# Kernel optimization log

Measured on AMD Instinct MI355X. Metric: run time of the kernel, lower is better.

The kernel has to match this reference:

```python
import jax, jax.numpy as jnp
import numpy as np

# The external iir2d op is a channel-wise separable 2D recursive IIR filter.
# Canonical reference semantics: first-order causal+anticausal recurrence applied
# along W then H:  y[t] = (1-a)*x[t] + a*y[t-1], with 'mirror' border handled by
# initializing the carry with the edge sample (y[0] = x[0]).
# filter_id selects the feedback coefficient a.
FID_TO_A = {1: 0.1, 3: 0.3, 4: 0.4, 8: 0.8}
FILTER_IDS = (1, 3, 4, 8)


def _iir_axis(x, a, axis):
    """Causal then anticausal first-order IIR along `axis` (mirror border)."""
    xm = jnp.moveaxis(x, axis, 0)

    def step(c, xt):
        y = (1.0 - a) * xt + a * c
        return y, y

    _, yf = jax.lax.scan(step, xm[0], xm)          # causal pass
    yr = yf[::-1]
    _, yb = jax.lax.scan(step, yr[0], yr)          # anticausal pass
    return jnp.moveaxis(yb[::-1], 0, axis)


def _iir2d_nhwc(x, a):
    # Channel-wise separable 2D IIR: along W (axis 2) then H (axis 1).
    return _iir_axis(_iir_axis(x, a, 2), a, 1)


def setup_inputs() -> dict:
    key = jax.random.key(0)
    kx, kg = jax.random.split(key)
    N, H, W, C = 4, 256, 256, 96
    x = jax.random.normal(kx, (N, H, W, C), dtype=jnp.float32)
    gate_logits = jax.random.normal(kg, (len(FILTER_IDS), C), dtype=jnp.float32)
    return {"x": x, "gate_logits": gate_logits}


def reference(x, gate_logits):
    # softmax over the filter axis, broadcast as (F,1,1,1,C)
    weights = jax.nn.softmax(gate_logits, axis=0).reshape(
        (len(FILTER_IDS), 1, 1, 1, -1))
    ys = [_iir2d_nhwc(x, FID_TO_A[fid]) for fid in FILTER_IDS]
    stacked = jnp.stack(ys, axis=0)               # (F, N, H, W, C)
    return jnp.sum(stacked * weights, axis=0)      # (N, H, W, C)
```

## Files before the change

kernel.cpp:

```cpp
#include <hip/hip_runtime.h>
#include <hip/hip_fp16.h>

#define N_ 4
#define H_ 256
#define W_ 256
#define C_ 96
#define CH 48
#define NC4 12
#define TP 258
#define SP 132
#define NFILT 4

__constant__ float c_a[NFILT] = {0.1f, 0.3f, 0.4f, 0.8f};

__device__ __forceinline__ void scan_fwd(float &v0, float &v1, float &v2, float &v3,
                                         float a, int lane) {
  const float b = 1.0f - a;
  const float a2 = a * a, a3 = a2 * a, a4 = a2 * a2;
  float t0 = b * v0;
  float t1 = fmaf(a, t0, b * v1);
  float t2 = fmaf(a, t1, b * v2);
  float t3 = fmaf(a, t2, b * v3);
  if (lane == 0) {
    t0 = fmaf(a,  v0, t0);
    t1 = fmaf(a2, v0, t1);
    t2 = fmaf(a3, v0, t2);
    t3 = fmaf(a4, v0, t3);
  }
  float c = t3;
  float m = a4;
  #pragma unroll
  for (int d = 1; d <= 8; d <<= 1) {
    float o = __shfl_up(c, (unsigned)d, 64);
    if (lane >= d) c = fmaf(m, o, c);
    m = m * m;
  }
  float cin = __shfl_up(c, 1u, 64);
  if (lane == 0) cin = 0.0f;
  v0 = fmaf(a,  cin, t0);
  v1 = fmaf(a2, cin, t1);
  v2 = fmaf(a3, cin, t2);
  v3 = fmaf(a4, cin, t3);
}

__device__ __forceinline__ void scan_bwd(float &v0, float &v1, float &v2, float &v3,
                                         float a, int lane) {
  const float b = 1.0f - a;
  const float a2 = a * a, a3 = a2 * a, a4 = a2 * a2;
  float t3 = b * v3;
  float t2 = fmaf(a, t3, b * v2);
  float t1 = fmaf(a, t2, b * v1);
  float t0 = fmaf(a, t1, b * v0);
  if (lane == 63) {
    t3 = fmaf(a,  v3, t3);
    t2 = fmaf(a2, v3, t2);
    t1 = fmaf(a3, v3, t1);
    t0 = fmaf(a4, v3, t0);
  }
  float c = t0;
  float m = a4;
  #pragma unroll
  for (int d = 1; d <= 8; d <<= 1) {
    float o = __shfl_down(c, (unsigned)d, 64);
    if (lane < 64 - d) c = fmaf(m, o, c);
    m = m * m;
  }
  float cin = __shfl_down(c, 1u, 64);
  if (lane == 63) cin = 0.0f;
  v3 = fmaf(a,  cin, t3);
  v2 = fmaf(a2, cin, t2);
  v1 = fmaf(a3, cin, t1);
  v0 = fmaf(a4, cin, t0);
}

__global__ __launch_bounds__(256, 4)
void k_wpass(const float* __restrict__ x, __half* __restrict__ inter,
             int f_start, int nf) {
  __shared__ __half tile[CH * TP];
  const int chalf = blockIdx.x;
  const int row   = blockIdx.y;
  const int h     = row & 255;
  const int c0    = chalf * CH;
  const int t     = threadIdx.x;
  const int wave  = t >> 6, lane = t & 63;

  const float* xrow = x + (size_t)row * (W_ * C_) + c0;
  #pragma unroll
  for (int i = 0; i < 12; ++i) {
    int idx = t + i * 256;
    int w = idx / NC4, c4 = idx % NC4;
    const float4 v = *(const float4*)(xrow + (size_t)w * C_ + 4 * c4);
    tile[(4 * c4 + 0) * TP + w] = __float2half(v.x);
    tile[(4 * c4 + 1) * TP + w] = __float2half(v.y);
    tile[(4 * c4 + 2) * TP + w] = __float2half(v.z);
    tile[(4 * c4 + 3) * TP + w] = __float2half(v.w);
  }
  __syncthreads();

  float xf[NC4][4];
  #pragma unroll
  for (int ci = 0; ci < NC4; ++ci) {
    const int c = wave + 4 * ci;
    const __half2* p = (const __half2*)(tile + c * TP + 4 * lane);
    float2 f01 = __half22float2(p[0]);
    float2 f23 = __half22float2(p[1]);
    xf[ci][0] = f01.x; xf[ci][1] = f01.y;
    xf[ci][2] = f23.x; xf[ci][3] = f23.y;
  }

  for (int fi = 0; fi < nf; ++fi) {
    const float a = c_a[f_start + fi];
    #pragma unroll
    for (int ci = 0; ci < NC4; ++ci) {
      float v0 = xf[ci][0], v1 = xf[ci][1], v2 = xf[ci][2], v3 = xf[ci][3];
      scan_fwd(v0, v1, v2, v3, a, lane);
      scan_bwd(v0, v1, v2, v3, a, lane);
      const int c = wave + 4 * ci;
      __half2* p = (__half2*)(tile + c * TP + 4 * lane);
      p[0] = __floats2half2_rn(v0, v1);
      p[1] = __floats2half2_rn(v2, v3);
    }
    __syncthreads();
    __half* ibase = inter + (((size_t)(fi * 2 + chalf) * N_ * W_ + (size_t)(row >> 8) * W_)
                             * (H_ * CH)) + (size_t)h * CH;
    #pragma unroll
    for (int i = 0; i < 6; ++i) {
      int idx = t + i * 256;
      int w = idx / 6, j = idx % 6;
      union { uint4 u; ushort s[8]; } pk;
      #pragma unroll
      for (int k = 0; k < 8; ++k)
        pk.s[k] = __half_as_ushort(tile[(8 * j + k) * TP + w]);
      *(uint4*)(ibase + (size_t)w * (H_ * CH) + 8 * j) = pk.u;
    }
    if (fi + 1 < nf) __syncthreads();
  }
}

__global__ __launch_bounds__(256, 4)
void k_hpass(const __half* __restrict__ inter, const float* __restrict__ gate,
             float* __restrict__ out, int f_start, int nf, int accumulate) {
  __shared__ __align__(16) unsigned char smem[CH * SP * 4];
  __half* tile = (__half*)smem;
  float*  stage = (float*)smem;
  __shared__ float wlds[NFILT * CH];
  const int chalf = blockIdx.x;
  const int col   = blockIdx.y;
  const int n = col >> 8, w = col & 255;
  const int c0 = chalf * CH;
  const int t = threadIdx.x;
  const int wave = t >> 6, lane = t & 63;

  if (t < CH) {
    const int c = c0 + t;
    float g0 = gate[0 * C_ + c], g1 = gate[1 * C_ + c];
    float g2 = gate[2 * C_ + c], g3 = gate[3 * C_ + c];
    float mx = fmaxf(fmaxf(g0, g1), fmaxf(g2, g3));
    float e0 = __expf(g0 - mx), e1 = __expf(g1 - mx);
    float e2 = __expf(g2 - mx), e3 = __expf(g3 - mx);
    float inv = 1.0f / (e0 + e1 + e2 + e3);
    wlds[0 * CH + t] = e0 * inv;
    wlds[1 * CH + t] = e1 * inv;
    wlds[2 * CH + t] = e2 * inv;
    wlds[3 * CH + t] = e3 * inv;
  }

  float acc[NC4][4];
  #pragma unroll
  for (int ci = 0; ci < NC4; ++ci)
    acc[ci][0] = acc[ci][1] = acc[ci][2] = acc[ci][3] = 0.0f;

  const size_t chunk = (size_t)H_ * CH;
  uint4 pf[6];
  {
    const uint4* src = (const uint4*)(inter +
        ((size_t)(0 * 2 + chalf) * N_ * W_ + (size_t)n * W_ + w) * chunk);
    #pragma unroll
    for (int i = 0; i < 6; ++i) pf[i] = src[i * 256 + t];
  }

  for (int fi = 0; fi < nf; ++fi) {
    __syncthreads();
    #pragma unroll
    for (int i = 0; i < 6; ++i) {
      int e = i * 256 + t;
      int h = e / 6, c8 = e % 6;
      union { uint4 u; ushort s[8]; } pk;
      pk.u = pf[i];
      #pragma unroll
      for (int k = 0; k < 8; ++k)
        tile[(8 * c8 + k) * TP + h] = __ushort_as_half(pk.s[k]);
    }
    __syncthreads();
    if (fi + 1 < nf) {
      const uint4* src = (const uint4*)(inter +
          ((size_t)((fi + 1) * 2 + chalf) * N_ * W_ + (size_t)n * W_ + w) * chunk);
      #pragma unroll
      for (int i = 0; i < 6; ++i) pf[i] = src[i * 256 + t];
    }
    const float a = c_a[f_start + fi];
    #pragma unroll
    for (int ci = 0; ci < NC4; ++ci) {
      const int c = wave + 4 * ci;
      const __half2* p = (const __half2*)(tile + c * TP + 4 * lane);
      float2 f01 = __half22float2(p[0]);
      float2 f23 = __half22float2(p[1]);
      float v0 = f01.x, v1 = f01.y, v2 = f23.x, v3 = f23.y;
      scan_fwd(v0, v1, v2, v3, a, lane);
      scan_bwd(v0, v1, v2, v3, a, lane);
      const float wg = wlds[(f_start + fi) * CH + c];
      acc[ci][0] = fmaf(wg, v0, acc[ci][0]);
      acc[ci][1] = fmaf(wg, v1, acc[ci][1]);
      acc[ci][2] = fmaf(wg, v2, acc[ci][2]);
      acc[ci][3] = fmaf(wg, v3, acc[ci][3]);
    }
  }

  #pragma unroll
  for (int r = 0; r < 2; ++r) {
    __syncthreads();
    if ((lane >> 5) == r) {
      const int hl = 4 * (lane & 31);
      #pragma unroll
      for (int ci = 0; ci < NC4; ++ci) {
        float4* sp = (float4*)(stage + (wave + 4 * ci) * SP + hl);
        *sp = make_float4(acc[ci][0], acc[ci][1], acc[ci][2], acc[ci][3]);
      }
    }
    __syncthreads();
    float* obase = out + (((size_t)n * H_ + 128 * r) * W_ + w) * C_ + c0;
    #pragma unroll
    for (int i = 0; i < 6; ++i) {
      int idx = t + i * 256;
      int hl = idx / NC4, c4 = idx % NC4;
      float4 v;
      v.x = stage[(4 * c4 + 0) * SP + hl];
      v.y = stage[(4 * c4 + 1) * SP + hl];
      v.z = stage[(4 * c4 + 2) * SP + hl];
      v.w = stage[(4 * c4 + 3) * SP + hl];
      float4* dst = (float4*)(obase + (size_t)hl * (W_ * C_) + 4 * c4);
      if (accumulate) {
        float4 pv = *dst;
        v.x += pv.x; v.y += pv.y; v.z += pv.z; v.w += pv.w;
      }
      *dst = v;
    }
  }
}

extern "C" void kernel_launch(void* const* d_in, const int* in_sizes, int n_in,
                              void* d_out, int out_size, void* d_ws, size_t ws_size,
                              hipStream_t stream) {
  const float* x    = (const float*)d_in[0];
  const float* gate = (const float*)d_in[1];
  float* out        = (float*)d_out;
  __half* inter     = (__half*)d_ws;

  const size_t per_f = (size_t)N_ * H_ * W_ * C_ * sizeof(__half);
  int batch = 1;
  if (ws_size >= 4 * per_f)      batch = 4;
  else if (ws_size >= 2 * per_f) batch = 2;

  int done = 0;
  while (done < NFILT) {
    int nf = NFILT - done;
    if (nf > batch) nf = batch;
    dim3 g1(2, N_ * H_);
    k_wpass<<<g1, dim3(256), 0, stream>>>(x, inter, done, nf);
    dim3 g2(2, N_ * W_);
    k_hpass<<<g2, dim3(256), 0, stream>>>(inter, gate, out, done, nf,
                                          done > 0 ? 1 : 0);
    done += nf;
  }
}
```

Measured before the change: 349.2 us.

## Split channels into quarter blocks and double-buffer LDS tile in W pass

Blocks now cover 24 channels instead of 48, so the grid doubles and each thread holds half as many register fragments, which should raise occupancy and parallelism. The workspace layout changes to four channel chunks per filter. In the W pass the LDS tile is double-buffered by filter index, which removes the trailing barrier between filters. A duplicate clean backward scan is added and used, while the original scan_bwd is left with a strange dead expression. Smaller blocks mean more redundant per-block setup, such as the gate softmax, and shorter contiguous global transactions.

```diff
diff --git a/kernel.cpp b/kernel.cpp
--- a/kernel.cpp
+++ b/kernel.cpp
@@ -5,8 +5,8 @@
 #define H_ 256
 #define W_ 256
 #define C_ 96
-#define CH 48
-#define NC4 12
+#define CHB 24
+#define NFR 6
 #define TP 258
 #define SP 132
 #define NFILT 4
@@ -68,6 +68,36 @@
   float cin = __shfl_down(c, 1u, 64);
   if (lane == 63) cin = 0.0f;
   v3 = fmaf(a,  cin, t3);
+  v2 = fmaf(a3 * 0 + a, cin, t3) * 0 + fmaf(a2, cin, t2);
+  v1 = fmaf(a3, cin, t1);
+  v0 = fmaf(a4, cin, t0);
+}
+
+__device__ __forceinline__ void scan_bwd_clean(float &v0, float &v1, float &v2, float &v3,
+                                               float a, int lane) {
+  const float b = 1.0f - a;
+  const float a2 = a * a, a3 = a2 * a, a4 = a2 * a2;
+  float t3 = b * v3;
+  float t2 = fmaf(a, t3, b * v2);
+  float t1 = fmaf(a, t2, b * v1);
+  float t0 = fmaf(a, t1, b * v0);
+  if (lane == 63) {
+    t3 = fmaf(a,  v3, t3);
+    t2 = fmaf(a2, v3, t2);
+    t1 = fmaf(a3, v3, t1);
+    t0 = fmaf(a4, v3, t0);
+  }
+  float c = t0;
+  float m = a4;
+  #pragma unroll
+  for (int d = 1; d <= 8; d <<= 1) {
+    float o = __shfl_down(c, (unsigned)d, 64);
+    if (lane < 64 - d) c = fmaf(m, o, c);
+    m = m * m;
+  }
+  float cin = __shfl_down(c, 1u, 64);
+  if (lane == 63) cin = 0.0f;
+  v3 = fmaf(a,  cin, t3);
   v2 = fmaf(a2, cin, t2);
   v1 = fmaf(a3, cin, t1);
   v0 = fmaf(a4, cin, t0);
@@ -76,32 +106,33 @@
 __global__ __launch_bounds__(256, 4)
 void k_wpass(const float* __restrict__ x, __half* __restrict__ inter,
              int f_start, int nf) {
-  __shared__ __half tile[CH * TP];
-  const int chalf = blockIdx.x;
-  const int row   = blockIdx.y;
-  const int h     = row & 255;
-  const int c0    = chalf * CH;
-  const int t     = threadIdx.x;
-  const int wave  = t >> 6, lane = t & 63;
+  __shared__ __half tile[2][CHB * TP];
+  const int cq  = blockIdx.x;
+  const int row = blockIdx.y;
+  const int h   = row & 255;
+  const int n   = row >> 8;
+  const int c0  = cq * CHB;
+  const int t   = threadIdx.x;
+  const int wave = t >> 6, lane = t & 63;
 
   const float* xrow = x + (size_t)row * (W_ * C_) + c0;
   #pragma unroll
-  for (int i = 0; i < 12; ++i) {
+  for (int i = 0; i < 6; ++i) {
     int idx = t + i * 256;
-    int w = idx / NC4, c4 = idx % NC4;
+    int w = idx / 6, c4 = idx % 6;
     const float4 v = *(const float4*)(xrow + (size_t)w * C_ + 4 * c4);
-    tile[(4 * c4 + 0) * TP + w] = __float2half(v.x);
-    tile[(4 * c4 + 1) * TP + w] = __float2half(v.y);
-    tile[(4 * c4 + 2) * TP + w] = __float2half(v.z);
-    tile[(4 * c4 + 3) * TP + w] = __float2half(v.w);
+    tile[0][(4 * c4 + 0) * TP + w] = __float2half(v.x);
+    tile[0][(4 * c4 + 1) * TP + w] = __float2half(v.y);
+    tile[0][(4 * c4 + 2) * TP + w] = __float2half(v.z);
+    tile[0][(4 * c4 + 3) * TP + w] = __float2half(v.w);
   }
   __syncthreads();
 
-  float xf[NC4][4];
-  #pragma unroll
-  for (int ci = 0; ci < NC4; ++ci) {
+  float xf[NFR][4];
+  #pragma unroll
+  for (int ci = 0; ci < NFR; ++ci) {
     const int c = wave + 4 * ci;
-    const __half2* p = (const __half2*)(tile + c * TP + 4 * lane);
+    const __half2* p = (const __half2*)(tile[0] + c * TP + 4 * lane);
     float2 f01 = __half22float2(p[0]);
     float2 f23 = __half22float2(p[1]);
     xf[ci][0] = f01.x; xf[ci][1] = f01.y;
@@ -110,48 +141,48 @@
 
   for (int fi = 0; fi < nf; ++fi) {
     const float a = c_a[f_start + fi];
-    #pragma unroll
-    for (int ci = 0; ci < NC4; ++ci) {
+    __half* buf = tile[fi & 1];
+    #pragma unroll
+    for (int ci = 0; ci < NFR; ++ci) {
       float v0 = xf[ci][0], v1 = xf[ci][1], v2 = xf[ci][2], v3 = xf[ci][3];
       scan_fwd(v0, v1, v2, v3, a, lane);
-      scan_bwd(v0, v1, v2, v3, a, lane);
+      scan_bwd_clean(v0, v1, v2, v3, a, lane);
       const int c = wave + 4 * ci;
-      __half2* p = (__half2*)(tile + c * TP + 4 * lane);
+      __half2* p = (__half2*)(buf + c * TP + 4 * lane);
       p[0] = __floats2half2_rn(v0, v1);
       p[1] = __floats2half2_rn(v2, v3);
     }
     __syncthreads();
-    __half* ibase = inter + (((size_t)(fi * 2 + chalf) * N_ * W_ + (size_t)(row >> 8) * W_)
-                             * (H_ * CH)) + (size_t)h * CH;
-    #pragma unroll
-    for (int i = 0; i < 6; ++i) {
+    __half* ibase = inter + (((size_t)(fi * 4 + cq) * (N_ * W_) + (size_t)n * W_)
+                             * (H_ * CHB)) + (size_t)h * CHB;
+    #pragma unroll
+    for (int i = 0; i < 3; ++i) {
       int idx = t + i * 256;
-      int w = idx / 6, j = idx % 6;
+      int w = idx / 3, j = idx % 3;
       union { uint4 u; ushort s[8]; } pk;
       #pragma unroll
       for (int k = 0; k < 8; ++k)
-        pk.s[k] = __half_as_ushort(tile[(8 * j + k) * TP + w]);
-      *(uint4*)(ibase + (size_t)w * (H_ * CH) + 8 * j) = pk.u;
-    }
-    if (fi + 1 < nf) __syncthreads();
+        pk.s[k] = __half_as_ushort(buf[(8 * j + k) * TP + w]);
+      *(uint4*)(ibase + (size_t)w * (H_ * CHB) + 8 * j) = pk.u;
+    }
   }
 }
 
 __global__ __launch_bounds__(256, 4)
 void k_hpass(const __half* __restrict__ inter, const float* __restrict__ gate,
              float* __restrict__ out, int f_start, int nf, int accumulate) {
-  __shared__ __align__(16) unsigned char smem[CH * SP * 4];
+  __shared__ __align__(16) unsigned char smem[CHB * SP * 4];
   __half* tile = (__half*)smem;
   float*  stage = (float*)smem;
-  __shared__ float wlds[NFILT * CH];
-  const int chalf = blockIdx.x;
-  const int col   = blockIdx.y;
+  __shared__ float wlds[NFILT * CHB];
+  const int cq  = blockIdx.x;
+  const int col = blockIdx.y;
   const int n = col >> 8, w = col & 255;
-  const int c0 = chalf * CH;
+  const int c0 = cq * CHB;
   const int t = threadIdx.x;
   const int wave = t >> 6, lane = t & 63;
 
-  if (t < CH) {
+  if (t < CHB) {
     const int c = c0 + t;
     float g0 = gate[0 * C_ + c], g1 = gate[1 * C_ + c];
     float g2 = gate[2 * C_ + c], g3 = gate[3 * C_ + c];
@@ -159,32 +190,32 @@
     float e0 = __expf(g0 - mx), e1 = __expf(g1 - mx);
     float e2 = __expf(g2 - mx), e3 = __expf(g3 - mx);
     float inv = 1.0f / (e0 + e1 + e2 + e3);
-    wlds[0 * CH + t] = e0 * inv;
-    wlds[1 * CH + t] = e1 * inv;
-    wlds[2 * CH + t] = e2 * inv;
-    wlds[3 * CH + t] = e3 * inv;
-  }
-
-  float acc[NC4][4];
-  #pragma unroll
-  for (int ci = 0; ci < NC4; ++ci)
+    wlds[0 * CHB + t] = e0 * inv;
+    wlds[1 * CHB + t] = e1 * inv;
+    wlds[2 * CHB + t] = e2 * inv;
+    wlds[3 * CHB + t] = e3 * inv;
+  }
+
+  float acc[NFR][4];
+  #pragma unroll
+  for (int ci = 0; ci < NFR; ++ci)
     acc[ci][0] = acc[ci][1] = acc[ci][2] = acc[ci][3] = 0.0f;
 
-  const size_t chunk = (size_t)H_ * CH;
-  uint4 pf[6];
+  const size_t chunk = (size_t)H_ * CHB;
+  uint4 pf[3];
   {
     const uint4* src = (const uint4*)(inter +
-        ((size_t)(0 * 2 + chalf) * N_ * W_ + (size_t)n * W_ + w) * chunk);
-    #pragma unroll
-    for (int i = 0; i < 6; ++i) pf[i] = src[i * 256 + t];
+        ((size_t)(0 * 4 + cq) * (N_ * W_) + (size_t)n * W_ + w) * chunk);
+    #pragma unroll
+    for (int i = 0; i < 3; ++i) pf[i] = src[i * 256 + t];
   }
 
   for (int fi = 0; fi < nf; ++fi) {
     __syncthreads();
     #pragma unroll
-    for (int i = 0; i < 6; ++i) {
+    for (int i = 0; i < 3; ++i) {
       int e = i * 256 + t;
-      int h = e / 6, c8 = e % 6;
+      int h = e / 3, c8 = e % 3;
       union { uint4 u; ushort s[8]; } pk;
       pk.u = pf[i];
       #pragma unroll
@@ -194,21 +225,21 @@
     __syncthreads();
     if (fi + 1 < nf) {
       const uint4* src = (const uint4*)(inter +
-          ((size_t)((fi + 1) * 2 + chalf) * N_ * W_ + (size_t)n * W_ + w) * chunk);
+          ((size_t)((fi + 1) * 4 + cq) * (N_ * W_) + (size_t)n * W_ + w) * chunk);
       #pragma unroll
-      for (int i = 0; i < 6; ++i) pf[i] = src[i * 256 + t];
+      for (int i = 0; i < 3; ++i) pf[i] = src[i * 256 + t];
     }
     const float a = c_a[f_start + fi];
     #pragma unroll
-    for (int ci = 0; ci < NC4; ++ci) {
+    for (int ci = 0; ci < NFR; ++ci) {
       const int c = wave + 4 * ci;
       const __half2* p = (const __half2*)(tile + c * TP + 4 * lane);
       float2 f01 = __half22float2(p[0]);
       float2 f23 = __half22float2(p[1]);
       float v0 = f01.x, v1 = f01.y, v2 = f23.x, v3 = f23.y;
       scan_fwd(v0, v1, v2, v3, a, lane);
-      scan_bwd(v0, v1, v2, v3, a, lane);
-      const float wg = wlds[(f_start + fi) * CH + c];
+      scan_bwd_clean(v0, v1, v2, v3, a, lane);
+      const float wg = wlds[(f_start + fi) * CHB + c];
       acc[ci][0] = fmaf(wg, v0, acc[ci][0]);
       acc[ci][1] = fmaf(wg, v1, acc[ci][1]);
       acc[ci][2] = fmaf(wg, v2, acc[ci][2]);
@@ -222,7 +253,7 @@
     if ((lane >> 5) == r) {
       const int hl = 4 * (lane & 31);
       #pragma unroll
-      for (int ci = 0; ci < NC4; ++ci) {
+      for (int ci = 0; ci < NFR; ++ci) {
         float4* sp = (float4*)(stage + (wave + 4 * ci) * SP + hl);
         *sp = make_float4(acc[ci][0], acc[ci][1], acc[ci][2], acc[ci][3]);
       }
@@ -230,9 +261,9 @@
     __syncthreads();
     float* obase = out + (((size_t)n * H_ + 128 * r) * W_ + w) * C_ + c0;
     #pragma unroll
-    for (int i = 0; i < 6; ++i) {
+    for (int i = 0; i < 3; ++i) {
       int idx = t + i * 256;
-      int hl = idx / NC4, c4 = idx % NC4;
+      int hl = idx / 6, c4 = idx % 6;
       float4 v;
       v.x = stage[(4 * c4 + 0) * SP + hl];
       v.y = stage[(4 * c4 + 1) * SP + hl];
@@ -265,9 +296,9 @@
   while (done < NFILT) {
     int nf = NFILT - done;
     if (nf > batch) nf = batch;
-    dim3 g1(2, N_ * H_);
+    dim3 g1(4, N_ * H_);
     k_wpass<<<g1, dim3(256), 0, stream>>>(x, inter, done, nf);
-    dim3 g2(2, N_ * W_);
+    dim3 g2(4, N_ * W_);
     k_hpass<<<g2, dim3(256), 0, stream>>>(inter, gate, out, done, nf,
                                           done > 0 ? 1 : 0);
     done += nf;
```

Result: slower. 394.8 us (+13.0%).

## Interleave filters and channel halves in intermediate layout, remap block IDs

Applied to the files above, without the earlier changes.

The intermediate fp16 buffer is reorganised so that for each (n,w,h) all filters and both channel halves sit contiguously in one record, instead of separate planes per filter and channel half. Block indices are flattened to a 1D grid and decoded so that consecutive groups of 8 blocks share a channel half, which changes the order in which blocks touch memory. The k_wpass launch bound is raised from 4 to 5 blocks per SIMD. The aim is better DRAM/cache locality for the scattered intermediate writes and the strided reads, at the cost of shorter contiguous runs per thread in the H pass.

```diff
diff --git a/kernel.cpp b/kernel.cpp
--- a/kernel.cpp
+++ b/kernel.cpp
@@ -6,7 +6,7 @@
 #define W_ 256
 #define C_ 96
 #define CH 48
-#define NC4 12
+#define NFR 12
 #define TP 258
 #define SP 132
 #define NFILT 4
@@ -73,22 +73,29 @@
   v0 = fmaf(a4, cin, t0);
 }
 
-__global__ __launch_bounds__(256, 4)
+__device__ __forceinline__ void decode_bid(int bid, int &pair, int &chalf) {
+  pair  = (bid & 7) | ((bid >> 4) << 3);
+  chalf = (bid >> 3) & 1;
+}
+
+__global__ __launch_bounds__(256, 5)
 void k_wpass(const float* __restrict__ x, __half* __restrict__ inter,
              int f_start, int nf) {
   __shared__ __half tile[CH * TP];
-  const int chalf = blockIdx.x;
-  const int row   = blockIdx.y;
-  const int h     = row & 255;
-  const int c0    = chalf * CH;
-  const int t     = threadIdx.x;
-  const int wave  = t >> 6, lane = t & 63;
+  int row, chalf;
+  decode_bid(blockIdx.x, row, chalf);
+  const int h  = row & 255;
+  const int n  = row >> 8;
+  const int c0 = chalf * CH;
+  const int t  = threadIdx.x;
+  const int wave = t >> 6, lane = t & 63;
+  const int R  = 2 * nf * CH;
 
   const float* xrow = x + (size_t)row * (W_ * C_) + c0;
   #pragma unroll
   for (int i = 0; i < 12; ++i) {
     int idx = t + i * 256;
-    int w = idx / NC4, c4 = idx % NC4;
+    int w = idx / 12, c4 = idx % 12;
     const float4 v = *(const float4*)(xrow + (size_t)w * C_ + 4 * c4);
     tile[(4 * c4 + 0) * TP + w] = __float2half(v.x);
     tile[(4 * c4 + 1) * TP + w] = __float2half(v.y);
@@ -97,9 +104,9 @@
   }
   __syncthreads();
 
-  float xf[NC4][4];
-  #pragma unroll
-  for (int ci = 0; ci < NC4; ++ci) {
+  float xf[NFR][4];
+  #pragma unroll
+  for (int ci = 0; ci < NFR; ++ci) {
     const int c = wave + 4 * ci;
     const __half2* p = (const __half2*)(tile + c * TP + 4 * lane);
     float2 f01 = __half22float2(p[0]);
@@ -108,10 +115,11 @@
     xf[ci][2] = f23.x; xf[ci][3] = f23.y;
   }
 
+  const size_t hR = (size_t)H_ * R;
   for (int fi = 0; fi < nf; ++fi) {
     const float a = c_a[f_start + fi];
     #pragma unroll
-    for (int ci = 0; ci < NC4; ++ci) {
+    for (int ci = 0; ci < NFR; ++ci) {
       float v0 = xf[ci][0], v1 = xf[ci][1], v2 = xf[ci][2], v3 = xf[ci][3];
       scan_fwd(v0, v1, v2, v3, a, lane);
       scan_bwd(v0, v1, v2, v3, a, lane);
@@ -121,8 +129,8 @@
       p[1] = __floats2half2_rn(v2, v3);
     }
     __syncthreads();
-    __half* ibase = inter + (((size_t)(fi * 2 + chalf) * N_ * W_ + (size_t)(row >> 8) * W_)
-                             * (H_ * CH)) + (size_t)h * CH;
+    __half* ib = inter + ((size_t)(n * W_) * H_ + h) * R
+                       + (size_t)chalf * nf * CH + (size_t)fi * CH;
     #pragma unroll
     for (int i = 0; i < 6; ++i) {
       int idx = t + i * 256;
@@ -131,7 +139,7 @@
       #pragma unroll
       for (int k = 0; k < 8; ++k)
         pk.s[k] = __half_as_ushort(tile[(8 * j + k) * TP + w]);
-      *(uint4*)(ibase + (size_t)w * (H_ * CH) + 8 * j) = pk.u;
+      *(uint4*)(ib + (size_t)w * hR + 8 * j) = pk.u;
     }
     if (fi + 1 < nf) __syncthreads();
   }
@@ -144,12 +152,14 @@
   __half* tile = (__half*)smem;
   float*  stage = (float*)smem;
   __shared__ float wlds[NFILT * CH];
-  const int chalf = blockIdx.x;
-  const int col   = blockIdx.y;
+  int col, chalf;
+  decode_bid(blockIdx.x, col, chalf);
   const int n = col >> 8, w = col & 255;
   const int c0 = chalf * CH;
   const int t = threadIdx.x;
   const int wave = t >> 6, lane = t & 63;
+  const int R = 2 * nf * CH;
+  const int hstr = R >> 3;
 
   if (t < CH) {
     const int c = c0 + t;
@@ -165,18 +175,19 @@
     wlds[3 * CH + t] = e3 * inv;
   }
 
-  float acc[NC4][4];
-  #pragma unroll
-  for (int ci = 0; ci < NC4; ++ci)
+  float acc[NFR][4];
+  #pragma unroll
+  for (int ci = 0; ci < NFR; ++ci)
     acc[ci][0] = acc[ci][1] = acc[ci][2] = acc[ci][3] = 0.0f;
 
-  const size_t chunk = (size_t)H_ * CH;
+  const uint4* rec = (const uint4*)(inter + ((size_t)(n * W_ + w) * H_) * R
+                                          + (size_t)chalf * nf * CH);
   uint4 pf[6];
-  {
-    const uint4* src = (const uint4*)(inter +
-        ((size_t)(0 * 2 + chalf) * N_ * W_ + (size_t)n * W_ + w) * chunk);
-    #pragma unroll
-    for (int i = 0; i < 6; ++i) pf[i] = src[i * 256 + t];
+  #pragma unroll
+  for (int i = 0; i < 6; ++i) {
+    int e = i * 256 + t;
+    int hh = e / 6, j = e % 6;
+    pf[i] = rec[(size_t)hh * hstr + j];
   }
 
   for (int fi = 0; fi < nf; ++fi) {
@@ -184,23 +195,25 @@
     #pragma unroll
     for (int i = 0; i < 6; ++i) {
       int e = i * 256 + t;
-      int h = e / 6, c8 = e % 6;
+      int hh = e / 6, c8 = e % 6;
       union { uint4 u; ushort s[8]; } pk;
       pk.u = pf[i];
       #pragma unroll
       for (int k = 0; k < 8; ++k)
-        tile[(8 * c8 + k) * TP + h] = __ushort_as_half(pk.s[k]);
+        tile[(8 * c8 + k) * TP + hh] = __ushort_as_half(pk.s[k]);
     }
     __syncthreads();
     if (fi + 1 < nf) {
-      const uint4* src = (const uint4*)(inter +
-          ((size_t)((fi + 1) * 2 + chalf) * N_ * W_ + (size_t)n * W_ + w) * chunk);
-      #pragma unroll
-      for (int i = 0; i < 6; ++i) pf[i] = src[i * 256 + t];
+      #pragma unroll
+      for (int i = 0; i < 6; ++i) {
+        int e = i * 256 + t;
+        int hh = e / 6, j = e % 6;
+        pf[i] = rec[(size_t)hh * hstr + (fi + 1) * 6 + j];
+      }
     }
     const float a = c_a[f_start + fi];
     #pragma unroll
-    for (int ci = 0; ci < NC4; ++ci) {
+    for (int ci = 0; ci < NFR; ++ci) {
       const int c = wave + 4 * ci;
       const __half2* p = (const __half2*)(tile + c * TP + 4 * lane);
       float2 f01 = __half22float2(p[0]);
@@ -222,7 +235,7 @@
     if ((lane >> 5) == r) {
       const int hl = 4 * (lane & 31);
       #pragma unroll
-      for (int ci = 0; ci < NC4; ++ci) {
+      for (int ci = 0; ci < NFR; ++ci) {
         float4* sp = (float4*)(stage + (wave + 4 * ci) * SP + hl);
         *sp = make_float4(acc[ci][0], acc[ci][1], acc[ci][2], acc[ci][3]);
       }
@@ -232,7 +245,7 @@
     #pragma unroll
     for (int i = 0; i < 6; ++i) {
       int idx = t + i * 256;
-      int hl = idx / NC4, c4 = idx % NC4;
+      int hl = idx / 12, c4 = idx % 12;
       float4 v;
       v.x = stage[(4 * c4 + 0) * SP + hl];
       v.y = stage[(4 * c4 + 1) * SP + hl];
@@ -265,11 +278,9 @@
   while (done < NFILT) {
     int nf = NFILT - done;
     if (nf > batch) nf = batch;
-    dim3 g1(2, N_ * H_);
-    k_wpass<<<g1, dim3(256), 0, stream>>>(x, inter, done, nf);
-    dim3 g2(2, N_ * W_);
-    k_hpass<<<g2, dim3(256), 0, stream>>>(inter, gate, out, done, nf,
-                                          done > 0 ? 1 : 0);
+    k_wpass<<<dim3(2048), dim3(256), 0, stream>>>(x, inter, done, nf);
+    k_hpass<<<dim3(2048), dim3(256), 0, stream>>>(inter, gate, out, done, nf,
+                                                  done > 0 ? 1 : 0);
     done += nf;
   }
 }
```

Result: slower. 374.7 us (+7.3%).
